# Optimization experiments

Hardware: AMD Instinct MI355X
Metric: run time of the kernel (lower is better)

The kernel has to match this reference:

```python
import jax, jax.numpy as jnp
import numpy as np

# Config constants from init_kwargs
DIM_GROUPS = [32, 32]   # hyper_cuts_dim_groups (sum == lsh_key_dim == d_key)
K_MAX = 64              # max candidates kept per query token


def _group_exact_match(qb, kb):
    """qb, kb: [B, L, d] binary {0,1} floats.
    Returns eq[b, i, j] = True iff all d bits of query i equal key j.
    Faithful to merge(Wu-Manber prefix match, Trie full-stride match):
    the Trie stores the full binary vector chunked by stride, so a Trie hit
    requires exact equality of the whole group's bit vector, which subsumes
    the Wu-Manber prefix condition; their intersection is exact equality.
    """
    # number of mismatching bits between query i and key j
    mism = (jnp.einsum('bid,bjd->bij', qb, 1.0 - kb)
            + jnp.einsum('bid,bjd->bij', 1.0 - qb, kb))
    return mism == 0.0


def setup_inputs() -> dict:
    key = jax.random.key(0)
    k1, k2 = jax.random.split(key)
    B, L, D = 4, 2048, 64
    return {
        'query_up': jax.random.normal(k1, (B, L, D), dtype=jnp.float32),
        'key_up': jax.random.normal(k2, (B, L, D), dtype=jnp.float32),
        'head_idx': 0,
    }


def reference(query_up, key_up, head_idx):
    B, L, _ = query_up.shape
    # binary_quantize: (x > 0).float()
    qb = (query_up > 0).astype(jnp.float32)
    kb = (key_up > 0).astype(jnp.float32)
    # per dim-group exact match (Wu-Manber \cap Trie), union across groups
    match = jnp.zeros((B, L, L), dtype=bool)
    start = 0
    for gd in DIM_GROUPS:
        match = match | _group_exact_match(qb[..., start:start + gd],
                                           kb[..., start:start + gd])
        start += gd
    # gather up to K_MAX smallest matching key indices per query, pad with -1
    idx = jnp.where(match, jnp.arange(L, dtype=jnp.int32)[None, None, :], L)
    cand = jnp.sort(idx, axis=-1)[..., :K_MAX]          # [B, L, K_MAX]
    return jnp.where(cand == L, -1, cand)
```

## Files before the change

### kernel.cpp

```cpp
#include <hip/hip_runtime.h>
#include <stdint.h>


#define LSEQ 2048
#define DDIM 64
#define KMAX 64
#define QPB  32
#define NW   16
#define GROUP 32

__global__ __launch_bounds__(1024) void cand_kernel(
    const float* __restrict__ query, const float* __restrict__ key,
    int* __restrict__ out) {
    __shared__ uint2 ks[LSEQ];

    const int bpb  = LSEQ / QPB;
    int b    = blockIdx.x / bpb;
    int qblk = blockIdx.x % bpb;
    int lane = threadIdx.x & 63;
    int wave = threadIdx.x >> 6;

    const float* kb = key + (size_t)b * LSEQ * DDIM;
    for (int g = 0; g < LSEQ / NW / GROUP; ++g) {
        float v[GROUP];
#pragma unroll
        for (int u = 0; u < GROUP; ++u) {
            int row = g * (NW * GROUP) + u * NW + wave;
            v[u] = kb[(size_t)row * DDIM + lane];
        }
        unsigned long long m[GROUP];
#pragma unroll
        for (int u = 0; u < GROUP; ++u)
            m[u] = __ballot(v[u] > 0.0f);
        if (lane == 0) {
#pragma unroll
            for (int u = 0; u < GROUP; ++u) {
                int row = g * (NW * GROUP) + u * NW + wave;
                ks[row] = make_uint2((unsigned)m[u], (unsigned)(m[u] >> 32));
            }
        }
    }

    const float* qb = query + ((size_t)b * LSEQ + (size_t)qblk * QPB) * DDIM;
    int q0 = wave * 2;
    float v0 = qb[(size_t)q0 * DDIM + lane];
    float v1 = qb[(size_t)(q0 + 1) * DDIM + lane];
    unsigned long long m0 = __ballot(v0 > 0.0f);
    unsigned long long m1 = __ballot(v1 > 0.0f);

    __syncthreads();

    unsigned long long below = (1ull << lane) - 1ull;
    for (int t = 0; t < 2; ++t) {
        unsigned long long qm = t ? m1 : m0;
        unsigned q1 = (unsigned)qm, q2 = (unsigned)(qm >> 32);
        int* obase =
            out + ((size_t)b * LSEQ + (size_t)qblk * QPB + q0 + t) * KMAX;

        unsigned long long acc = 0;
        int cnt = 0;
#pragma unroll
        for (int c = 0; c < LSEQ / 64; ++c) {
            uint2 kv = ks[c * 64 + lane];
            bool m = (kv.x == q1) || (kv.y == q2);
            unsigned long long mask = __ballot(m);
            acc |= mask;
            cnt += __popcll(mask);
        }

        if (acc != 0) {
            int c2 = 0;
            for (int c = 0; c < LSEQ / 64; ++c) {
                uint2 kv = ks[c * 64 + lane];
                bool m = (kv.x == q1) || (kv.y == q2);
                unsigned long long mask = __ballot(m);
                if (m) {
                    int pos = c2 + __popcll(mask & below);
                    if (pos < KMAX) obase[pos] = c * 64 + lane;
                }
                c2 += __popcll(mask);
            }
        }
        if (lane >= cnt) obase[lane] = -1;
    }
}

extern "C" void kernel_launch(void* const* d_in, const int* in_sizes, int n_in,
                              void* d_out, int out_size, void* d_ws, size_t ws_size,
                              hipStream_t stream) {
    const float* q = (const float*)d_in[0];
    const float* k = (const float*)d_in[1];
    int* out = (int*)d_out;

    int total = in_sizes[0];
    int B = total / (LSEQ * DDIM);

    cand_kernel<<<B * (LSEQ / QPB), 1024, 0, stream>>>(q, k, out);
}
```

Before: 72.57 us.

## Split key signature computation into separate kernel and match from global workspace

```diff
diff --git a/kernel.cpp b/kernel.cpp
--- a/kernel.cpp
+++ b/kernel.cpp
@@ -5,58 +5,129 @@
 #define LSEQ 2048
 #define DDIM 64
 #define KMAX 64
+#define RPW  8
+
+__global__ __launch_bounds__(256) void sig_kernel(
+    const float* __restrict__ key, uint2* __restrict__ ksig, int nrows) {
+    int wid  = (int)((blockIdx.x * blockDim.x + threadIdx.x) >> 6);
+    int lane = threadIdx.x & 63;
+    int row0 = wid * RPW;
+    if (row0 >= nrows) return;
+    const float* base = key + (size_t)row0 * DDIM + lane;
+    float v[RPW];
+#pragma unroll
+    for (int u = 0; u < RPW; ++u)
+        v[u] = base[(size_t)u * DDIM];
+    unsigned long long m[RPW];
+#pragma unroll
+    for (int u = 0; u < RPW; ++u)
+        m[u] = __ballot(v[u] > 0.0f);
+    if (lane == 0) {
+#pragma unroll
+        for (int u = 0; u < RPW; ++u)
+            ksig[row0 + u] = make_uint2((unsigned)m[u], (unsigned)(m[u] >> 32));
+    }
+}
+
+__global__ __launch_bounds__(256) void match_kernel(
+    const float* __restrict__ query, const uint2* __restrict__ ksig,
+    int* __restrict__ out, int nq) {
+    int wid  = (int)((blockIdx.x * blockDim.x + threadIdx.x) >> 6);
+    int lane = threadIdx.x & 63;
+    int q0 = wid * 2;
+    if (q0 >= nq) return;
+    int b = q0 >> 11;
+
+    const float* qp = query + (size_t)q0 * DDIM + lane;
+    float v0 = qp[0], v1 = qp[DDIM];
+    unsigned long long qm0 = __ballot(v0 > 0.0f);
+    unsigned long long qm1 = __ballot(v1 > 0.0f);
+    unsigned a0 = (unsigned)qm0, g0 = (unsigned)(qm0 >> 32);
+    unsigned a1 = (unsigned)qm1, g1 = (unsigned)(qm1 >> 32);
+
+    const uint4* kt = (const uint4*)(ksig + (size_t)b * LSEQ) + lane;
+    unsigned long long acc0 = 0, acc1 = 0;
+    int cnt0 = 0, cnt1 = 0;
+#pragma unroll
+    for (int i = 0; i < LSEQ / 128; ++i) {
+        uint4 kv = kt[(size_t)i * 64];
+        bool mA0 = (kv.x == a0) | (kv.y == g0);
+        bool mB0 = (kv.z == a0) | (kv.w == g0);
+        bool mA1 = (kv.x == a1) | (kv.y == g1);
+        bool mB1 = (kv.z == a1) | (kv.w == g1);
+        unsigned long long s;
+        s = __ballot(mA0); acc0 |= s; cnt0 += __popcll(s);
+        s = __ballot(mB0); acc0 |= s; cnt0 += __popcll(s);
+        s = __ballot(mA1); acc1 |= s; cnt1 += __popcll(s);
+        s = __ballot(mB1); acc1 |= s; cnt1 += __popcll(s);
+    }
+
+    int* o0 = out + (size_t)q0 * KMAX;
+    int* o1 = o0 + KMAX;
+
+    if (acc0 | acc1) {
+        const uint2* ks = ksig + (size_t)b * LSEQ;
+        unsigned long long below = (1ull << lane) - 1ull;
+        for (int t = 0; t < 2; ++t) {
+            unsigned qa = t ? a1 : a0, qg = t ? g1 : g0;
+            int* ob = t ? o1 : o0;
+            int c2 = 0;
+            for (int c = 0; c < LSEQ / 64; ++c) {
+                uint2 kv = ks[c * 64 + lane];
+                bool m = (kv.x == qa) || (kv.y == qg);
+                unsigned long long mask = __ballot(m);
+                if (m) {
+                    int pos = c2 + __popcll(mask & below);
+                    if (pos < KMAX) ob[pos] = c * 64 + lane;
+                }
+                c2 += __popcll(mask);
+            }
+        }
+    }
+    if (lane >= cnt0) o0[lane] = -1;
+    if (lane >= cnt1) o1[lane] = -1;
+}
+
 #define QPB  32
 #define NW   16
 #define GROUP 32
-
-__global__ __launch_bounds__(1024) void cand_kernel(
+__global__ __launch_bounds__(1024) void fused_kernel(
     const float* __restrict__ query, const float* __restrict__ key,
     int* __restrict__ out) {
     __shared__ uint2 ks[LSEQ];
-
     const int bpb  = LSEQ / QPB;
     int b    = blockIdx.x / bpb;
     int qblk = blockIdx.x % bpb;
     int lane = threadIdx.x & 63;
     int wave = threadIdx.x >> 6;
-
     const float* kb = key + (size_t)b * LSEQ * DDIM;
     for (int g = 0; g < LSEQ / NW / GROUP; ++g) {
         float v[GROUP];
 #pragma unroll
-        for (int u = 0; u < GROUP; ++u) {
-            int row = g * (NW * GROUP) + u * NW + wave;
-            v[u] = kb[(size_t)row * DDIM + lane];
-        }
+        for (int u = 0; u < GROUP; ++u)
+            v[u] = kb[(size_t)(g * (NW * GROUP) + u * NW + wave) * DDIM + lane];
         unsigned long long m[GROUP];
 #pragma unroll
-        for (int u = 0; u < GROUP; ++u)
-            m[u] = __ballot(v[u] > 0.0f);
+        for (int u = 0; u < GROUP; ++u) m[u] = __ballot(v[u] > 0.0f);
         if (lane == 0) {
 #pragma unroll
-            for (int u = 0; u < GROUP; ++u) {
-                int row = g * (NW * GROUP) + u * NW + wave;
-                ks[row] = make_uint2((unsigned)m[u], (unsigned)(m[u] >> 32));
-            }
+            for (int u = 0; u < GROUP; ++u)
+                ks[g * (NW * GROUP) + u * NW + wave] =
+                    make_uint2((unsigned)m[u], (unsigned)(m[u] >> 32));
         }
     }
-
     const float* qb = query + ((size_t)b * LSEQ + (size_t)qblk * QPB) * DDIM;
     int q0 = wave * 2;
     float v0 = qb[(size_t)q0 * DDIM + lane];
     float v1 = qb[(size_t)(q0 + 1) * DDIM + lane];
     unsigned long long m0 = __ballot(v0 > 0.0f);
     unsigned long long m1 = __ballot(v1 > 0.0f);
-
     __syncthreads();
-
     unsigned long long below = (1ull << lane) - 1ull;
     for (int t = 0; t < 2; ++t) {
         unsigned long long qm = t ? m1 : m0;
         unsigned q1 = (unsigned)qm, q2 = (unsigned)(qm >> 32);
-        int* obase =
-            out + ((size_t)b * LSEQ + (size_t)qblk * QPB + q0 + t) * KMAX;
-
+        int* obase = out + ((size_t)b * LSEQ + (size_t)qblk * QPB + q0 + t) * KMAX;
         unsigned long long acc = 0;
         int cnt = 0;
 #pragma unroll
@@ -64,10 +135,8 @@
             uint2 kv = ks[c * 64 + lane];
             bool m = (kv.x == q1) || (kv.y == q2);
             unsigned long long mask = __ballot(m);
-            acc |= mask;
-            cnt += __popcll(mask);
+            acc |= mask; cnt += __popcll(mask);
         }
-
         if (acc != 0) {
             int c2 = 0;
             for (int c = 0; c < LSEQ / 64; ++c) {
@@ -94,6 +163,15 @@
 
     int total = in_sizes[0];
     int B = total / (LSEQ * DDIM);
+    int nrows = B * LSEQ;
 
-    cand_kernel<<<B * (LSEQ / QPB), 1024, 0, stream>>>(q, k, out);
+    if (ws_size >= (size_t)nrows * sizeof(uint2)) {
+        uint2* ksig = (uint2*)d_ws;
+        int sig_waves = nrows / RPW;
+        sig_kernel<<<sig_waves * 64 / 256, 256, 0, stream>>>(k, ksig, nrows);
+        int match_waves = nrows / 2;
+        match_kernel<<<match_waves * 64 / 256, 256, 0, stream>>>(q, ksig, out, nrows);
+    } else {
+        fused_kernel<<<B * (LSEQ / QPB), 1024, 0, stream>>>(q, k, out);
+    }
 }
```

After: 63.29 us. 12.8% less time.

## Process more queries per block and read two keys per lane in the count pass

Applied to the files above, without the earlier changes.

```diff
diff --git a/kernel.cpp b/kernel.cpp
--- a/kernel.cpp
+++ b/kernel.cpp
@@ -5,11 +5,12 @@
 #define LSEQ 2048
 #define DDIM 64
 #define KMAX 64
-#define QPB  32
+#define QPB  128
 #define NW   16
 #define GROUP 32
+#define QG   8
 
-__global__ __launch_bounds__(1024) void cand_kernel(
+__global__ __launch_bounds__(1024) void fused_kernel(
     const float* __restrict__ query, const float* __restrict__ key,
     int* __restrict__ out) {
     __shared__ uint2 ks[LSEQ];
@@ -24,64 +25,65 @@
     for (int g = 0; g < LSEQ / NW / GROUP; ++g) {
         float v[GROUP];
 #pragma unroll
-        for (int u = 0; u < GROUP; ++u) {
-            int row = g * (NW * GROUP) + u * NW + wave;
-            v[u] = kb[(size_t)row * DDIM + lane];
-        }
+        for (int u = 0; u < GROUP; ++u)
+            v[u] = kb[(size_t)(g * (NW * GROUP) + u * NW + wave) * DDIM + lane];
         unsigned long long m[GROUP];
 #pragma unroll
         for (int u = 0; u < GROUP; ++u)
             m[u] = __ballot(v[u] > 0.0f);
         if (lane == 0) {
 #pragma unroll
-            for (int u = 0; u < GROUP; ++u) {
-                int row = g * (NW * GROUP) + u * NW + wave;
-                ks[row] = make_uint2((unsigned)m[u], (unsigned)(m[u] >> 32));
-            }
+            for (int u = 0; u < GROUP; ++u)
+                ks[g * (NW * GROUP) + u * NW + wave] =
+                    make_uint2((unsigned)m[u], (unsigned)(m[u] >> 32));
         }
     }
 
     const float* qb = query + ((size_t)b * LSEQ + (size_t)qblk * QPB) * DDIM;
-    int q0 = wave * 2;
-    float v0 = qb[(size_t)q0 * DDIM + lane];
-    float v1 = qb[(size_t)(q0 + 1) * DDIM + lane];
-    unsigned long long m0 = __ballot(v0 > 0.0f);
-    unsigned long long m1 = __ballot(v1 > 0.0f);
+    int q0 = wave * QG;
+    float qv[QG];
+#pragma unroll
+    for (int u = 0; u < QG; ++u)
+        qv[u] = qb[(size_t)(q0 + u) * DDIM + lane];
+    unsigned long long qm[QG];
+#pragma unroll
+    for (int u = 0; u < QG; ++u)
+        qm[u] = __ballot(qv[u] > 0.0f);
 
     __syncthreads();
 
+    const uint4* kt4 = (const uint4*)ks;
     unsigned long long below = (1ull << lane) - 1ull;
-    for (int t = 0; t < 2; ++t) {
-        unsigned long long qm = t ? m1 : m0;
-        unsigned q1 = (unsigned)qm, q2 = (unsigned)(qm >> 32);
-        int* obase =
-            out + ((size_t)b * LSEQ + (size_t)qblk * QPB + q0 + t) * KMAX;
+    for (int t = 0; t < QG; ++t) {
+        unsigned qa = (unsigned)qm[t], qg = (unsigned)(qm[t] >> 32);
+        int* ob = out + ((size_t)b * LSEQ + (size_t)qblk * QPB + q0 + t) * KMAX;
 
         unsigned long long acc = 0;
         int cnt = 0;
 #pragma unroll
-        for (int c = 0; c < LSEQ / 64; ++c) {
-            uint2 kv = ks[c * 64 + lane];
-            bool m = (kv.x == q1) || (kv.y == q2);
-            unsigned long long mask = __ballot(m);
-            acc |= mask;
-            cnt += __popcll(mask);
+        for (int i = 0; i < LSEQ / 128; ++i) {
+            uint4 kv = kt4[i * 64 + lane];
+            bool mA = (kv.x == qa) | (kv.y == qg);
+            bool mB = (kv.z == qa) | (kv.w == qg);
+            unsigned long long s;
+            s = __ballot(mA); acc |= s; cnt += __popcll(s);
+            s = __ballot(mB); acc |= s; cnt += __popcll(s);
         }
 
         if (acc != 0) {
             int c2 = 0;
             for (int c = 0; c < LSEQ / 64; ++c) {
                 uint2 kv = ks[c * 64 + lane];
-                bool m = (kv.x == q1) || (kv.y == q2);
+                bool m = (kv.x == qa) || (kv.y == qg);
                 unsigned long long mask = __ballot(m);
                 if (m) {
                     int pos = c2 + __popcll(mask & below);
-                    if (pos < KMAX) obase[pos] = c * 64 + lane;
+                    if (pos < KMAX) ob[pos] = c * 64 + lane;
                 }
                 c2 += __popcll(mask);
             }
         }
-        if (lane >= cnt) obase[lane] = -1;
+        if (lane >= cnt) ob[lane] = -1;
     }
 }
 
@@ -95,5 +97,5 @@
     int total = in_sizes[0];
     int B = total / (LSEQ * DDIM);
 
-    cand_kernel<<<B * (LSEQ / QPB), 1024, 0, stream>>>(q, k, out);
+    fused_kernel<<<B * (LSEQ / QPB), 1024, 0, stream>>>(q, k, out);
 }
```

Result: slower. 81.41 us (+12.2%).
